# Kernel optimization log

Measured on AMD Instinct MI355X. Metric: run time of the kernel, lower is better.

## Reference

```python
import jax, jax.numpy as jnp
from jax import lax
import numpy as np

EPS = 1e-9

def squash(x):
    # squash along last axis: ||x||^2/(1+||x||^2) * x/||x||
    mag_sq = jnp.sum(x * x, axis=-1, keepdims=True)
    mag = jnp.sqrt(mag_sq + EPS)
    return mag_sq / (1.0 + mag_sq) * (x / (mag + EPS))

def setup_inputs() -> dict:
    key = jax.random.key(0)
    ks = jax.random.split(key, 4)
    x = jax.random.normal(ks[0], (64, 1, 64, 64), jnp.float32)
    conv1_w = jax.random.normal(ks[1], (64, 1, 5, 5), jnp.float32) * 0.1
    conv1_b = jnp.zeros((64,), jnp.float32)
    prim_w = jax.random.normal(ks[2], (64, 64, 9, 9), jnp.float32) * 0.05
    prim_b = jnp.zeros((64,), jnp.float32)
    # DigitCaps W: (num_routes=8*28*28, num_caps=10, out_dim=16, in_dim=8); torch uses randn
    W = jax.random.normal(ks[3], (6272, 10, 16, 8), jnp.float32)
    return {"x": x, "conv1_w": conv1_w, "conv1_b": conv1_b,
            "prim_w": prim_w, "prim_b": prim_b, "W": W}

def reference(x, conv1_w, conv1_b, prim_w, prim_b, W):
    dn = ("NCHW", "OIHW", "NCHW")
    # ConvLayer: conv(1->64, k5, pad2) + relu, spatial preserved
    h = lax.conv_general_dilated(x, conv1_w, (1, 1), [(2, 2), (2, 2)], dimension_numbers=dn)
    h = jax.nn.relu(h + conv1_b[None, :, None, None])
    # PrimaryCaps: 8 convs (64->8, k9, s2) fused as one 64-channel conv
    u = lax.conv_general_dilated(h, prim_w, (2, 2), "VALID", dimension_numbers=dn)
    u = u + prim_b[None, :, None, None]  # (B, 64, 28, 28)
    B, _, H, Wd = u.shape
    # (B, caps=8, dim=8, H, W) -> (B, caps, H, W, dim) -> (B, caps*H*W, 8)
    u = u.reshape(B, 8, 8, H, Wd).transpose(0, 1, 3, 4, 2).reshape(B, -1, 8)
    u = squash(u)
    # u_hat[b,n,o,i] = W[n,o,i,j] @ u[b,n,j]   (B, routes, 10, 16)
    u_hat = jnp.einsum("noij,bnj->bnoi", W, u)
    b_ij = jnp.zeros(u_hat.shape[:3], u_hat.dtype)  # (B, routes, 10)
    v = None
    for it in range(3):
        c = jax.nn.softmax(b_ij, axis=2)
        s = jnp.einsum("bno,bnoi->boi", c, u_hat)  # (B, 10, 16)
        v = squash(s)
        if it < 2:
            b_ij = b_ij + jnp.einsum("bnoi,boi->bno", u_hat, v)
    return v.reshape(B, -1)  # (B, 160)
```

## Files before the change

### kernel.cpp

```cpp
#include <hip/hip_runtime.h>
#include <math.h>

typedef unsigned short ushort_t;
typedef __attribute__((ext_vector_type(8))) short bf16x8;
typedef __attribute__((ext_vector_type(4))) float f32x4;
typedef __attribute__((ext_vector_type(8))) unsigned short us8;

typedef __attribute__((address_space(1))) unsigned int gu32;
typedef __attribute__((address_space(3))) unsigned int lu32;

__device__ __forceinline__ void gload16(const void* g, void* l) {
    __builtin_amdgcn_global_load_lds((const gu32*)g, (lu32*)l, 16, 0, 0);
}

__device__ __forceinline__ unsigned short f2bf(float f) {
    unsigned u = __float_as_uint(f);
    unsigned r = ((u >> 16) & 1u) + 0x7fffu;
    return (unsigned short)((u + r) >> 16);
}

#define HB_OFF    0ULL
#define WT2_OFF   8388608ULL
#define TMP_OFF   8554496ULL
#define UTB_OFF   11765760ULL
#define V0_OFF    13381632ULL
#define V1_OFF    13391872ULL
#define PART_OFF  13402112ULL
#define PART2_OFF 21430272ULL
#define WB2_OFF   21594112ULL

__global__ __launch_bounds__(256) void conv1_nhwc_kernel(const float* __restrict__ x,
                                                         const float* __restrict__ w,
                                                         const float* __restrict__ bias,
                                                         ushort_t* __restrict__ hb) {
    int t = blockIdx.x * 256 + threadIdx.x;
    int xx = t & 63, yy = (t >> 6) & 63, b = t >> 12;
    int cg = blockIdx.y;
    const float* xb = x + (size_t)b * 4096;
    float xv[25];
    #pragma unroll
    for (int ky = 0; ky < 5; ++ky) {
        int iy = yy + ky - 2;
        #pragma unroll
        for (int kx = 0; kx < 5; ++kx) {
            int ix = xx + kx - 2;
            bool ok = (iy >= 0 && iy < 64 && ix >= 0 && ix < 64);
            xv[ky * 5 + kx] = ok ? xb[iy * 64 + ix] : 0.f;
        }
    }
    us8 o;
    #pragma unroll
    for (int cc = 0; cc < 8; ++cc) {
        int c = cg * 8 + cc;
        float acc = bias[c];
        const float* wc = w + c * 25;
        #pragma unroll
        for (int k = 0; k < 25; ++k) acc = fmaf(xv[k], wc[k], acc);
        o[cc] = f2bf(fmaxf(acc, 0.f));
    }
    *(us8*)&hb[(size_t)t * 64 + cg * 8] = o;
}

__global__ __launch_bounds__(256) void prep_weights_kernel(const float* __restrict__ pw,
                                                           const float* __restrict__ W,
                                                           ushort_t* __restrict__ wt2,
                                                           ushort_t* __restrict__ Wb) {
    int bid = blockIdx.x;
    int tid = threadIdx.x;
    if (bid < 1296) {
        int t = bid * 256 + tid;
        int ic = t & 63, c = (t >> 6) & 63, p = t >> 12;
        wt2[t] = f2bf(pw[(size_t)(c * 64 + ic) * 81 + p]);
    } else {
        int t = (bid - 1296) * 256 + tid;
        const float* src = W + (size_t)t * 8;
        us8 o;
        #pragma unroll
        for (int j = 0; j < 8; ++j) o[j] = f2bf(src[j]);
        *(us8*)&Wb[(size_t)t * 8] = o;
    }
}

__global__ __launch_bounds__(256) void conv2_mfma_kernel(const ushort_t* __restrict__ hb,
                                                         const ushort_t* __restrict__ wt2,
                                                         const float* __restrict__ pb,
                                                         float* __restrict__ tmp) {
    __shared__ ushort_t As[3][4096];
    __shared__ ushort_t Bs[3][4096];

    int tid = threadIdx.x;
    int w = tid >> 6, lane = tid & 63;
    int m0 = blockIdx.x * 64;

    int srow = w * 16 + (lane >> 3);
    int srcchunk = (lane & 7) ^ ((lane >> 3) & 7);
    unsigned gbaseA[2];
    #pragma unroll
    for (int k = 0; k < 2; ++k) {
        int r = srow + k * 8;
        int m = m0 + r;
        int b = m / 784, pos = m % 784;
        int oy = pos / 28, ox = pos % 28;
        gbaseA[k] = ((unsigned)((b * 64 + 2 * oy) * 64 + 2 * ox)) * 64 + srcchunk * 8;
    }
    unsigned gbaseB[2] = { (unsigned)srow * 64 + srcchunk * 8,
                           (unsigned)(srow + 8) * 64 + srcchunk * 8 };

    int fr = lane & 15, fq = lane >> 4;
    int rlow = fr & 7;
    int c0 = (fq ^ rlow) * 8;
    int c1 = ((4 + fq) ^ rlow) * 8;
    int rowA = w * 16 + fr;
    int offA0 = rowA * 64 + c0, offA1 = rowA * 64 + c1;
    int offB0[4], offB1[4];
    #pragma unroll
    for (int jf = 0; jf < 4; ++jf) {
        int rowB = jf * 16 + fr;
        offB0[jf] = rowB * 64 + c0;
        offB1[jf] = rowB * 64 + c1;
    }

    f32x4 acc[4] = {};

    auto stage = [&](int p) {
        int slot = p % 3;
        int ky = p / 9, kx = p % 9;
        unsigned koff = (unsigned)(ky * 4096 + kx * 64);
        unsigned boff = (unsigned)p * 4096;
        gload16(hb + gbaseA[0] + koff, &As[slot][w * 1024]);
        gload16(hb + gbaseA[1] + koff, &As[slot][w * 1024 + 512]);
        gload16(wt2 + boff + gbaseB[0], &Bs[slot][w * 1024]);
        gload16(wt2 + boff + gbaseB[1], &Bs[slot][w * 1024 + 512]);
    };

    auto tap = [&](int p) {
        const ushort_t* A = As[p % 3];
        const ushort_t* B = Bs[p % 3];
        bf16x8 a0 = *(const bf16x8*)&A[offA0];
        bf16x8 a1 = *(const bf16x8*)&A[offA1];
        bf16x8 b0[4], b1[4];
        #pragma unroll
        for (int jf = 0; jf < 4; ++jf) {
            b0[jf] = *(const bf16x8*)&B[offB0[jf]];
            b1[jf] = *(const bf16x8*)&B[offB1[jf]];
        }
        #pragma unroll
        for (int jf = 0; jf < 4; ++jf)
            acc[jf] = __builtin_amdgcn_mfma_f32_16x16x32_bf16(a0, b0[jf], acc[jf], 0, 0, 0);
        #pragma unroll
        for (int jf = 0; jf < 4; ++jf)
            acc[jf] = __builtin_amdgcn_mfma_f32_16x16x32_bf16(a1, b1[jf], acc[jf], 0, 0, 0);
    };

    stage(0); stage(1); stage(2);

    for (int p = 0; p < 78; ++p) {
        asm volatile("s_waitcnt vmcnt(8)" ::: "memory");
        __builtin_amdgcn_s_barrier();
        __builtin_amdgcn_sched_barrier(0);
        tap(p);
        __builtin_amdgcn_sched_barrier(0);
        __builtin_amdgcn_s_barrier();
        stage(p + 3);
    }
    asm volatile("s_waitcnt vmcnt(8)" ::: "memory");
    __builtin_amdgcn_s_barrier();
    __builtin_amdgcn_sched_barrier(0);
    tap(78);
    asm volatile("s_waitcnt vmcnt(4)" ::: "memory");
    __builtin_amdgcn_s_barrier();
    __builtin_amdgcn_sched_barrier(0);
    tap(79);
    asm volatile("s_waitcnt vmcnt(0)" ::: "memory");
    __builtin_amdgcn_s_barrier();
    __builtin_amdgcn_sched_barrier(0);
    tap(80);

    #pragma unroll
    for (int jf = 0; jf < 4; ++jf) {
        int n = jf * 16 + fr;
        float bv = pb[n];
        #pragma unroll
        for (int reg = 0; reg < 4; ++reg) {
            int m = w * 16 + fq * 4 + reg;
            tmp[(size_t)(m0 + m) * 64 + n] = acc[jf][reg] + bv;
        }
    }
}

__global__ __launch_bounds__(256) void squash_u_kernel(const float* __restrict__ tmp,
                                                       ushort_t* __restrict__ utb) {
    int idx = blockIdx.x * 256 + threadIdx.x;
    int b = idx & 63;
    int n = idx >> 6;
    int caps = n / 784, pos = n % 784;
    const float* tp = tmp + ((size_t)b * 784 + pos) * 64 + caps * 8;
    float v[8]; float msq = 0.f;
    #pragma unroll
    for (int j = 0; j < 8; ++j) { v[j] = tp[j]; msq = fmaf(v[j], v[j], msq); }
    float mag = sqrtf(msq + 1e-9f);
    float sc = msq / (1.f + msq) / (mag + 1e-9f);
    us8 o;
    #pragma unroll
    for (int j = 0; j < 8; ++j) o[j] = f2bf(v[j] * sc);
    *(us8*)&utb[(size_t)idx * 8] = o;
}

#define RPB 8
__global__ __launch_bounds__(256) void routing_iter0_kernel(const ushort_t* __restrict__ Wb,
                                                            const ushort_t* __restrict__ utb,
                                                            float* __restrict__ part) {
    __shared__ ushort_t Wl[RPB * 1280];
    __shared__ ushort_t Ul[RPB * 512];
    int tid = threadIdx.x;
    int lane = tid & 63;
    int wid = tid >> 6;
    int fr = lane & 15, fq = lane >> 4;
    int n0 = blockIdx.x * RPB;

    {
        int w64 = wid * 64;
        const ushort_t* wsrc = Wb + (size_t)n0 * 1280;
        #pragma unroll
        for (int k = 0; k < 5; ++k)
            gload16(wsrc + (size_t)(k * 256 + tid) * 8, &Wl[(k * 256 + w64) * 8]);
        const ushort_t* usrc = utb + (size_t)n0 * 512;
        #pragma unroll
        for (int k = 0; k < 2; ++k)
            gload16(usrc + (size_t)(k * 256 + tid) * 8, &Ul[(k * 256 + w64) * 8]);
    }
    __syncthreads();

    f32x4 s4[10] = {};
    #pragma unroll
    for (int g = 0; g < 2; ++g) {
        int t = g * 4 + fq;
        bf16x8 bfrag = *(const bf16x8*)&Ul[(t * 64 + wid * 16 + fr) * 8];
        #pragma unroll
        for (int o = 0; o < 10; ++o) {
            bf16x8 afrag = *(const bf16x8*)&Wl[(t * 160 + o * 16 + fr) * 8];
            s4[o] = __builtin_amdgcn_mfma_f32_16x16x32_bf16(afrag, bfrag, s4[o], 0, 0, 0);
        }
    }

    float* pp = part + (size_t)blockIdx.x * 10240;
    int b = wid * 16 + fr;
    #pragma unroll
    for (int o = 0; o < 10; ++o)
        #pragma unroll
        for (int r = 0; r < 4; ++r)
            pp[(o * 16 + fq * 4 + r) * 64 + b] = s4[o][r];
}

template<int ITER>
__global__ __launch_bounds__(256) void routing5_kernel(const ushort_t* __restrict__ Wb,
                                                       const ushort_t* __restrict__ utb,
                                                       const float* __restrict__ v0,
                                                       const float* __restrict__ v1,
                                                       float* __restrict__ part) {
    __shared__ ushort_t Wl[RPB * 1280];
    __shared__ ushort_t Ul[RPB * 512];
    int tid = threadIdx.x;
    int lane = tid & 63;
    int wid = tid >> 6;
    int fr = lane & 15, fq = lane >> 4;
    int n0 = blockIdx.x * RPB;
    int b = wid * 16 + fr;

    {
        int w64 = wid * 64;
        const ushort_t* wsrc = Wb + (size_t)n0 * 1280;
        #pragma unroll
        for (int k = 0; k < 5; ++k)
            gload16(wsrc + (size_t)(k * 256 + tid) * 8, &Wl[(k * 256 + w64) * 8]);
        const ushort_t* usrc = utb + (size_t)n0 * 512;
        #pragma unroll
        for (int k = 0; k < 2; ++k)
            gload16(usrc + (size_t)(k * 256 + tid) * 8, &Ul[(k * 256 + w64) * 8]);
    }

    float vsum[40];
    #pragma unroll
    for (int o = 0; o < 10; ++o) {
        f32x4 a = *(const f32x4*)&v0[b * 160 + o * 16 + fq * 4];
        if (ITER == 2) {
            f32x4 cc = *(const f32x4*)&v1[b * 160 + o * 16 + fq * 4];
            a = a + cc;
        }
        *(f32x4*)&vsum[o * 4] = a;
    }

    __syncthreads();

    float sacc[40];
    #pragma unroll
    for (int q = 0; q < 40; ++q) sacc[q] = 0.f;

    const bf16x8 zf = {};
    const f32x4 zc = {};

    #pragma unroll 1
    for (int t = 0; t < RPB; ++t) {
        bf16x8 bfrag = zf;
        if (fq == 0) bfrag = *(const bf16x8*)&Ul[(t * 64 + b) * 8];

        f32x4 uh[10];
        #pragma unroll
        for (int o = 0; o < 10; ++o) {
            bf16x8 afrag = zf;
            if (fq == 0) afrag = *(const bf16x8*)&Wl[(t * 160 + o * 16 + fr) * 8];
            uh[o] = __builtin_amdgcn_mfma_f32_16x16x32_bf16(afrag, bfrag, zc, 0, 0, 0);
        }

        float c10[10];
        {
            float l[10];
            #pragma unroll
            for (int o = 0; o < 10; ++o) {
                float lo = uh[o][0] * vsum[o * 4] + uh[o][1] * vsum[o * 4 + 1] +
                           uh[o][2] * vsum[o * 4 + 2] + uh[o][3] * vsum[o * 4 + 3];
                lo += __shfl_xor(lo, 16);
                lo += __shfl_xor(lo, 32);
                l[o] = lo;
            }
            float m = l[0];
            #pragma unroll
            for (int o = 1; o < 10; ++o) m = fmaxf(m, l[o]);
            float sum = 0.f;
            #pragma unroll
            for (int o = 0; o < 10; ++o) { c10[o] = __expf(l[o] - m); sum += c10[o]; }
            float inv = 1.f / sum;
            #pragma unroll
            for (int o = 0; o < 10; ++o) c10[o] *= inv;
        }

        #pragma unroll
        for (int o = 0; o < 10; ++o) {
            float co = c10[o];
            sacc[o * 4 + 0] = fmaf(co, uh[o][0], sacc[o * 4 + 0]);
            sacc[o * 4 + 1] = fmaf(co, uh[o][1], sacc[o * 4 + 1]);
            sacc[o * 4 + 2] = fmaf(co, uh[o][2], sacc[o * 4 + 2]);
            sacc[o * 4 + 3] = fmaf(co, uh[o][3], sacc[o * 4 + 3]);
        }
    }

    float* pp = part + (size_t)blockIdx.x * 10240;
    #pragma unroll
    for (int o = 0; o < 10; ++o)
        #pragma unroll
        for (int r = 0; r < 4; ++r)
            pp[(o * 16 + fq * 4 + r) * 64 + b] = sacc[o * 4 + r];
}

__global__ __launch_bounds__(256) void reduce_part1_kernel(const float* __restrict__ part,
                                                           float* __restrict__ part2) {
    int idx = blockIdx.x * 256 + threadIdx.x;
    int kc = blockIdx.y;
    const float* p = part + (size_t)kc * 49 * 10240 + idx;
    float a0 = 0.f, a1 = 0.f, a2 = 0.f, a3 = 0.f;
    #pragma unroll
    for (int k = 0; k < 48; k += 4) {
        a0 += p[(size_t)(k + 0) * 10240];
        a1 += p[(size_t)(k + 1) * 10240];
        a2 += p[(size_t)(k + 2) * 10240];
        a3 += p[(size_t)(k + 3) * 10240];
    }
    part2[kc * 10240 + idx] = ((a0 + a1) + (a2 + a3)) + p[48ULL * 10240];
}

__global__ __launch_bounds__(256) void reduce_squash_kernel(const float* __restrict__ part2,
                                                            float scale,
                                                            float* __restrict__ v) {
    __shared__ float sv[16][17];
    int tid = threadIdx.x;
    int o = blockIdx.x;
    int i = tid >> 4, bl = tid & 15;
    int b = blockIdx.y * 16 + bl;
    int idx = (o * 16 + i) * 64 + b;
    float a0 = 0.f, a1 = 0.f, a2 = 0.f, a3 = 0.f;
    #pragma unroll
    for (int k = 0; k < 16; k += 4) {
        a0 += part2[(k + 0) * 10240 + idx];
        a1 += part2[(k + 1) * 10240 + idx];
        a2 += part2[(k + 2) * 10240 + idx];
        a3 += part2[(k + 3) * 10240 + idx];
    }
    float s = ((a0 + a1) + (a2 + a3)) * scale;
    sv[i][bl] = s * s;
    __syncthreads();
    float msq = 0.f;
    #pragma unroll
    for (int ii = 0; ii < 16; ++ii) msq += sv[ii][bl];
    float mag = sqrtf(msq + 1e-9f);
    float sc = msq / (1.f + msq) / (mag + 1e-9f);
    v[b * 160 + o * 16 + i] = s * sc;
}

extern "C" void kernel_launch(void* const* d_in, const int* in_sizes, int n_in,
                              void* d_out, int out_size, void* d_ws, size_t ws_size,
                              hipStream_t stream) {
    const float* x  = (const float*)d_in[0];
    const float* w1 = (const float*)d_in[1];
    const float* b1 = (const float*)d_in[2];
    const float* pw = (const float*)d_in[3];
    const float* pb = (const float*)d_in[4];
    const float* W  = (const float*)d_in[5];
    float* out = (float*)d_out;
    float* ws  = (float*)d_ws;

    ushort_t* hb    = (ushort_t*)(ws + HB_OFF);
    ushort_t* wt2   = (ushort_t*)(ws + WT2_OFF);
    float*    tmp   = ws + TMP_OFF;
    ushort_t* utb   = (ushort_t*)(ws + UTB_OFF);
    float*    v0    = ws + V0_OFF;
    float*    v1    = ws + V1_OFF;
    float*    part  = ws + PART_OFF;
    float*    part2 = ws + PART2_OFF;
    ushort_t* Wb    = (ushort_t*)(ws + WB2_OFF);

    prep_weights_kernel<<<5216, 256, 0, stream>>>(pw, W, wt2, Wb);
    conv1_nhwc_kernel<<<dim3(1024, 8), 256, 0, stream>>>(x, w1, b1, hb);
    conv2_mfma_kernel<<<784, 256, 0, stream>>>(hb, wt2, pb, tmp);
    squash_u_kernel<<<1568, 256, 0, stream>>>(tmp, utb);

    routing_iter0_kernel<<<784, 256, 0, stream>>>(Wb, utb, part);
    reduce_part1_kernel<<<dim3(40, 16), 256, 0, stream>>>(part, part2);
    reduce_squash_kernel<<<dim3(10, 4), 256, 0, stream>>>(part2, 0.1f, v0);

    routing5_kernel<1><<<784, 256, 0, stream>>>(Wb, utb, v0, nullptr, part);
    reduce_part1_kernel<<<dim3(40, 16), 256, 0, stream>>>(part, part2);
    reduce_squash_kernel<<<dim3(10, 4), 256, 0, stream>>>(part2, 1.f, v1);

    routing5_kernel<2><<<784, 256, 0, stream>>>(Wb, utb, v0, v1, part);
    reduce_part1_kernel<<<dim3(40, 16), 256, 0, stream>>>(part, part2);
    reduce_squash_kernel<<<dim3(10, 4), 256, 0, stream>>>(part2, 1.f, out);
}
```

Measured before the change: 325.7 us.

## Fuse primary-capsule squash into conv2 epilogue and switch to double buffering

The conv2 MFMA kernel now applies the bias, computes each 8-element capsule's squash via lane shuffles, and writes bf16 capsules directly in the routing layout. This removes the fp32 intermediate buffer and the separate squash kernel launch. The LDS pipeline is simplified from three stages with explicit vmcnt waits to two buffers with __syncthreads. That may expose more global-load latency, and the epilogue now does scattered 2-byte stores.

```diff
diff --git a/kernel.cpp b/kernel.cpp
--- a/kernel.cpp
+++ b/kernel.cpp
@@ -21,7 +21,6 @@
 
 #define HB_OFF    0ULL
 #define WT2_OFF   8388608ULL
-#define TMP_OFF   8554496ULL
 #define UTB_OFF   11765760ULL
 #define V0_OFF    13381632ULL
 #define V1_OFF    13391872ULL
@@ -84,9 +83,9 @@
 __global__ __launch_bounds__(256) void conv2_mfma_kernel(const ushort_t* __restrict__ hb,
                                                          const ushort_t* __restrict__ wt2,
                                                          const float* __restrict__ pb,
-                                                         float* __restrict__ tmp) {
-    __shared__ ushort_t As[3][4096];
-    __shared__ ushort_t Bs[3][4096];
+                                                         ushort_t* __restrict__ utb) {
+    __shared__ ushort_t As[2][4096];
+    __shared__ ushort_t Bs[2][4096];
 
     int tid = threadIdx.x;
     int w = tid >> 6, lane = tid & 63;
@@ -122,20 +121,24 @@
 
     f32x4 acc[4] = {};
 
-    auto stage = [&](int p) {
-        int slot = p % 3;
+    auto stage = [&](int p, int buf) {
         int ky = p / 9, kx = p % 9;
         unsigned koff = (unsigned)(ky * 4096 + kx * 64);
         unsigned boff = (unsigned)p * 4096;
-        gload16(hb + gbaseA[0] + koff, &As[slot][w * 1024]);
-        gload16(hb + gbaseA[1] + koff, &As[slot][w * 1024 + 512]);
-        gload16(wt2 + boff + gbaseB[0], &Bs[slot][w * 1024]);
-        gload16(wt2 + boff + gbaseB[1], &Bs[slot][w * 1024 + 512]);
+        gload16(hb + gbaseA[0] + koff, &As[buf][w * 1024]);
+        gload16(hb + gbaseA[1] + koff, &As[buf][w * 1024 + 512]);
+        gload16(wt2 + boff + gbaseB[0], &Bs[buf][w * 1024]);
+        gload16(wt2 + boff + gbaseB[1], &Bs[buf][w * 1024 + 512]);
     };
 
-    auto tap = [&](int p) {
-        const ushort_t* A = As[p % 3];
-        const ushort_t* B = Bs[p % 3];
+    stage(0, 0);
+    __syncthreads();
+
+    for (int p = 0; p < 81; ++p) {
+        int cur = p & 1;
+        if (p < 80) stage(p + 1, cur ^ 1);
+        const ushort_t* A = As[cur];
+        const ushort_t* B = Bs[cur];
         bf16x8 a0 = *(const bf16x8*)&A[offA0];
         bf16x8 a1 = *(const bf16x8*)&A[offA1];
         bf16x8 b0[4], b1[4];
@@ -150,60 +153,31 @@
         #pragma unroll
         for (int jf = 0; jf < 4; ++jf)
             acc[jf] = __builtin_amdgcn_mfma_f32_16x16x32_bf16(a1, b1[jf], acc[jf], 0, 0, 0);
-    };
-
-    stage(0); stage(1); stage(2);
-
-    for (int p = 0; p < 78; ++p) {
-        asm volatile("s_waitcnt vmcnt(8)" ::: "memory");
-        __builtin_amdgcn_s_barrier();
-        __builtin_amdgcn_sched_barrier(0);
-        tap(p);
-        __builtin_amdgcn_sched_barrier(0);
-        __builtin_amdgcn_s_barrier();
-        stage(p + 3);
-    }
-    asm volatile("s_waitcnt vmcnt(8)" ::: "memory");
-    __builtin_amdgcn_s_barrier();
-    __builtin_amdgcn_sched_barrier(0);
-    tap(78);
-    asm volatile("s_waitcnt vmcnt(4)" ::: "memory");
-    __builtin_amdgcn_s_barrier();
-    __builtin_amdgcn_sched_barrier(0);
-    tap(79);
-    asm volatile("s_waitcnt vmcnt(0)" ::: "memory");
-    __builtin_amdgcn_s_barrier();
-    __builtin_amdgcn_sched_barrier(0);
-    tap(80);
-
-    #pragma unroll
-    for (int jf = 0; jf < 4; ++jf) {
-        int n = jf * 16 + fr;
-        float bv = pb[n];
-        #pragma unroll
-        for (int reg = 0; reg < 4; ++reg) {
-            int m = w * 16 + fq * 4 + reg;
-            tmp[(size_t)(m0 + m) * 64 + n] = acc[jf][reg] + bv;
-        }
-    }
-}
-
-__global__ __launch_bounds__(256) void squash_u_kernel(const float* __restrict__ tmp,
-                                                       ushort_t* __restrict__ utb) {
-    int idx = blockIdx.x * 256 + threadIdx.x;
-    int b = idx & 63;
-    int n = idx >> 6;
-    int caps = n / 784, pos = n % 784;
-    const float* tp = tmp + ((size_t)b * 784 + pos) * 64 + caps * 8;
-    float v[8]; float msq = 0.f;
-    #pragma unroll
-    for (int j = 0; j < 8; ++j) { v[j] = tp[j]; msq = fmaf(v[j], v[j], msq); }
-    float mag = sqrtf(msq + 1e-9f);
-    float sc = msq / (1.f + msq) / (mag + 1e-9f);
-    us8 o;
-    #pragma unroll
-    for (int j = 0; j < 8; ++j) o[j] = f2bf(v[j] * sc);
-    *(us8*)&utb[(size_t)idx * 8] = o;
+        __syncthreads();
+    }
+
+    float bv[4];
+    #pragma unroll
+    for (int jf = 0; jf < 4; ++jf) bv[jf] = pb[jf * 16 + fr];
+
+    #pragma unroll
+    for (int reg = 0; reg < 4; ++reg) {
+        int m = m0 + w * 16 + fq * 4 + reg;
+        int bb = m / 784, pos = m % 784;
+        #pragma unroll
+        for (int jf = 0; jf < 4; ++jf) {
+            float val = acc[jf][reg] + bv[jf];
+            float v2 = val * val;
+            v2 += __shfl_xor(v2, 1);
+            v2 += __shfl_xor(v2, 2);
+            v2 += __shfl_xor(v2, 4);
+            float mag = sqrtf(v2 + 1e-9f);
+            float sc = v2 / (1.f + v2) / (mag + 1e-9f);
+            int g = jf * 2 + (fr >> 3);
+            int j = fr & 7;
+            utb[(size_t)((g * 784 + pos) * 64 + bb) * 8 + j] = f2bf(val * sc);
+        }
+    }
 }
 
 #define RPB 8
@@ -410,7 +384,6 @@
 
     ushort_t* hb    = (ushort_t*)(ws + HB_OFF);
     ushort_t* wt2   = (ushort_t*)(ws + WT2_OFF);
-    float*    tmp   = ws + TMP_OFF;
     ushort_t* utb   = (ushort_t*)(ws + UTB_OFF);
     float*    v0    = ws + V0_OFF;
     float*    v1    = ws + V1_OFF;
@@ -420,8 +393,7 @@
 
     prep_weights_kernel<<<5216, 256, 0, stream>>>(pw, W, wt2, Wb);
     conv1_nhwc_kernel<<<dim3(1024, 8), 256, 0, stream>>>(x, w1, b1, hb);
-    conv2_mfma_kernel<<<784, 256, 0, stream>>>(hb, wt2, pb, tmp);
-    squash_u_kernel<<<1568, 256, 0, stream>>>(tmp, utb);
+    conv2_mfma_kernel<<<784, 256, 0, stream>>>(hb, wt2, pb, utb);
 
     routing_iter0_kernel<<<784, 256, 0, stream>>>(Wb, utb, part);
     reduce_part1_kernel<<<dim3(40, 16), 256, 0, stream>>>(part, part2);
```

After: 290.1 us. -10.9%, faster.
